# Kernel tuning notes

Hardware: AMD Instinct MI355X
Metric: run time of the kernel (lower is better)

## Reference

```python
import jax, jax.numpy as jnp
import numpy as np

N = 8192       # tokens = batch x seq
D = 2048       # d_model
H = 2048       # per-expert hidden size
E = 8          # num_experts
TOP_K = 2


def setup_inputs() -> dict:
    key = jax.random.key(0)
    ks = jax.random.split(key, 6)
    x = jax.random.normal(ks[0], (N, D), dtype=jnp.float32)
    expert_weights = jax.random.uniform(ks[1], (N, TOP_K), dtype=jnp.float32)
    expert_indices = jax.random.randint(ks[2], (N, TOP_K), 0, E, dtype=jnp.int32)
    batch_size_per_expert = jnp.bincount(expert_indices.reshape(-1), length=E).astype(jnp.int32)
    scale = 0.02
    w1 = jax.random.normal(ks[3], (E, D, H), dtype=jnp.float32) * scale
    w2 = jax.random.normal(ks[4], (E, H, D), dtype=jnp.float32) * scale
    w3 = jax.random.normal(ks[5], (E, D, H), dtype=jnp.float32) * scale
    return {"x": x, "expert_weights": expert_weights, "expert_indices": expert_indices,
            "batch_size_per_expert": batch_size_per_expert, "w1": w1, "w2": w2, "w3": w3}


def reference(x, expert_weights, expert_indices, batch_size_per_expert, w1, w2, w3):
    """Math-equivalent to ParallelMLP.forward_once (non-EP path):
    sort tokens by expert, run per-expert SwiGLU MLP, unpermute and combine
    with top-k routing weights. Output does not depend on the sort order,
    so we express it as: out[t] = sum_k w[t,k] * expert_{idx[t,k]}(x[t]).
    """
    n, d = x.shape
    e = w1.shape[0]
    # Dense combine weights (n, E): scatter top-k routing weights.
    cw = jnp.zeros((n, e), x.dtype).at[jnp.arange(n)[:, None], expert_indices].add(expert_weights)
    out = jnp.zeros_like(x)
    for i in range(e):  # small fixed expert count
        h = jax.nn.silu(x @ w1[i]) * (x @ w3[i])  # (n, H) SwiGLU
        out = out + cw[:, i:i + 1] * (h @ w2[i])
    return out
```

## Files before the change

kernel.cpp:

```cpp
#include <hip/hip_runtime.h>
#include <stdint.h>

typedef unsigned short u16;
typedef __attribute__((ext_vector_type(8))) short s16x8;
typedef __attribute__((ext_vector_type(8))) unsigned short u16x8;
typedef __attribute__((ext_vector_type(4))) float f32x4;

#define N_TOK 8192
#define DDIM 2048
#define HDIM 2048
#define NEXP 8
#define NROWS 16384
#define MAXTILES 136

#define W1T_OFF    0ull
#define W3T_OFF    67108864ull
#define W2T_OFF    134217728ull
#define XBF_OFF    201326592ull
#define HBUF_OFF   234881024ull
#define RES_OFF    301989888ull
#define ROWTOK_OFF 369098752ull
#define POS_OFF    369168384ull
#define META_OFF   369233920ull
#define WS_NEED    369234048ull

__device__ __forceinline__ u16 f2bf(float f) {
  union { float f; unsigned u; } v; v.f = f;
  unsigned r = v.u + 0x7fffu + ((v.u >> 16) & 1u);
  return (u16)(r >> 16);
}
__device__ __forceinline__ float bf2f(u16 u) {
  union { unsigned u; float f; } v; v.u = ((unsigned)u) << 16; return v.f;
}
__device__ __forceinline__ void gload_lds16(const u16* g, u16* l) {
  __builtin_amdgcn_global_load_lds(
      (const __attribute__((address_space(1))) unsigned int*)g,
      (__attribute__((address_space(3))) unsigned int*)l, 16, 0, 0);
}

__global__ void r1_kernel(const int* __restrict__ bsz, int* __restrict__ meta,
                          int* __restrict__ rowtok) {
  if (threadIdx.x == 0) {
    int off = 0, tbv = 0;
    meta[8] = 0; meta[17] = 0;
    for (int e = 0; e < 8; ++e) {
      meta[e] = 0;
      int c = bsz[e];
      off += c;  meta[9 + e] = off;
      tbv += (c + 127) >> 7; meta[18 + e] = tbv;
    }
  }
  for (int p = 16384 + (int)threadIdx.x; p < 17408; p += 256) rowtok[p] = 0;
}

__global__ void r2_kernel(const int* __restrict__ eidx, int* __restrict__ meta,
                          int* __restrict__ rowtok, int* __restrict__ posOf) {
  int i = blockIdx.x * 256 + threadIdx.x;
  int e = eidx[i];
  int p = atomicAdd(&meta[e], 1);
  int row = meta[8 + e] + p;
  rowtok[row] = i >> 1;
  posOf[i] = row;
}

__global__ void convert_x_kernel(const float* __restrict__ x, u16* __restrict__ xbf) {
  long long c = blockIdx.x * 256 + threadIdx.x;
  const float4 v0 = *(const float4*)&x[c * 8];
  const float4 v1 = *(const float4*)&x[c * 8 + 4];
  u16x8 u;
  u[0] = f2bf(v0.x); u[1] = f2bf(v0.y); u[2] = f2bf(v0.z); u[3] = f2bf(v0.w);
  u[4] = f2bf(v1.x); u[5] = f2bf(v1.y); u[6] = f2bf(v1.z); u[7] = f2bf(v1.w);
  *(u16x8*)&xbf[c * 8] = u;
}

__global__ __launch_bounds__(256) void transpose_cvt_kernel(
    const float* __restrict__ w1, const float* __restrict__ w2, const float* __restrict__ w3,
    u16* __restrict__ w1T, u16* __restrict__ w2T, u16* __restrict__ w3T) {
  __shared__ float tile[64][65];
  int z = blockIdx.z;
  const float* src; u16* dst;
  if (z < 8)        { src = w1 + (size_t)z * 4194304;        dst = w1T + (size_t)z * 4194304; }
  else if (z < 16)  { src = w3 + (size_t)(z - 8) * 4194304;  dst = w3T + (size_t)(z - 8) * 4194304; }
  else              { src = w2 + (size_t)(z - 16) * 4194304; dst = w2T + (size_t)(z - 16) * 4194304; }
  int r0 = blockIdx.y * 64, c0 = blockIdx.x * 64;
  int tid = threadIdx.x;
  int lr = tid >> 4, lc4 = (tid & 15) * 4;
#pragma unroll
  for (int i = 0; i < 4; ++i) {
    const float4 v = *(const float4*)&src[(size_t)(r0 + lr + i * 16) * 2048 + c0 + lc4];
    tile[lr + i * 16][lc4 + 0] = v.x; tile[lr + i * 16][lc4 + 1] = v.y;
    tile[lr + i * 16][lc4 + 2] = v.z; tile[lr + i * 16][lc4 + 3] = v.w;
  }
  __syncthreads();
  int orb = tid >> 3, oc8 = (tid & 7) * 8;
#pragma unroll
  for (int i = 0; i < 2; ++i) {
    int orow = orb + i * 32;
    u16x8 u;
#pragma unroll
    for (int j = 0; j < 8; ++j) u[j] = f2bf(tile[oc8 + j][orow]);
    *(u16x8*)&dst[(size_t)(c0 + orow) * 2048 + r0 + oc8] = u;
  }
}

__global__ __launch_bounds__(256, 2) void gemm1_kernel(
    const u16* __restrict__ xbf, const u16* __restrict__ w1T, const u16* __restrict__ w3T,
    const int* __restrict__ rowtok, const int* __restrict__ meta, u16* __restrict__ hbuf) {
  const int* offs = meta + 8;
  const int* tb = meta + 17;
  const int tileId = blockIdx.x;
  if (tileId >= tb[8]) return;
  int e = 0;
#pragma unroll
  for (int q = 1; q < 8; ++q) if (tileId >= tb[q]) e = q;
  const int row0 = offs[e] + (tileId - tb[e]) * 128;
  const int vr = offs[e + 1] - row0;
  const int n0 = blockIdx.y * 128;

  __shared__ u16 lds[2][3][128 * 32];

  const int tid = threadIdx.x;
  const int wv = tid >> 6, lane = tid & 63;
  const int ra0 = tid >> 2, ca0 = (tid & 3) * 8;
  const int tokA0 = rowtok[row0 + ra0];
  const int tokA1 = rowtok[row0 + ra0 + 64];
  const u16* aS0 = xbf + (size_t)tokA0 * DDIM + ca0;
  const u16* aS1 = xbf + (size_t)tokA1 * DDIM + ca0;
  const u16* b1S0 = w1T + ((size_t)e * HDIM + n0 + ra0) * DDIM + ca0;
  const u16* b1S1 = b1S0 + (size_t)64 * DDIM;
  const u16* b3S0 = w3T + ((size_t)e * HDIM + n0 + ra0) * DDIM + ca0;
  const u16* b3S1 = b3S0 + (size_t)64 * DDIM;
  const int wub0 = wv * 512, wub1 = 2048 + wv * 512;

  f32x4 zero4 = {0.f, 0.f, 0.f, 0.f};
  f32x4 acc1[4][4], acc3[4][4];
#pragma unroll
  for (int m = 0; m < 4; ++m)
#pragma unroll
    for (int n = 0; n < 4; ++n) { acc1[m][n] = zero4; acc3[m][n] = zero4; }

#define STAGE1(bufi, kt) do { int k0_ = (kt) * 32; \
    gload_lds16(aS0 + k0_,  &lds[bufi][0][wub0]); \
    gload_lds16(aS1 + k0_,  &lds[bufi][0][wub1]); \
    gload_lds16(b1S0 + k0_, &lds[bufi][1][wub0]); \
    gload_lds16(b1S1 + k0_, &lds[bufi][1][wub1]); \
    gload_lds16(b3S0 + k0_, &lds[bufi][2][wub0]); \
    gload_lds16(b3S1 + k0_, &lds[bufi][2][wub1]); } while (0)

  STAGE1(0, 0);
  __syncthreads();

  const int lm = lane & 15, kg = lane >> 4;
  const int wr = (wv >> 1) * 64, wc = (wv & 1) * 64;

  for (int kt = 0; kt < 64; ++kt) {
    const int cur = kt & 1;
    if (kt + 1 < 64) STAGE1(cur ^ 1, kt + 1);
    s16x8 a[4], b1[4], b3[4];
#pragma unroll
    for (int m = 0; m < 4; ++m)
      a[m] = *(const s16x8*)&lds[cur][0][(wr + m * 16 + lm) * 32 + kg * 8];
#pragma unroll
    for (int n = 0; n < 4; ++n) {
      b1[n] = *(const s16x8*)&lds[cur][1][(wc + n * 16 + lm) * 32 + kg * 8];
      b3[n] = *(const s16x8*)&lds[cur][2][(wc + n * 16 + lm) * 32 + kg * 8];
    }
#pragma unroll
    for (int m = 0; m < 4; ++m)
#pragma unroll
      for (int n = 0; n < 4; ++n) {
        acc1[m][n] = __builtin_amdgcn_mfma_f32_16x16x32_bf16(a[m], b1[n], acc1[m][n], 0, 0, 0);
        acc3[m][n] = __builtin_amdgcn_mfma_f32_16x16x32_bf16(a[m], b3[n], acc3[m][n], 0, 0, 0);
      }
    __syncthreads();
  }

#pragma unroll
  for (int m = 0; m < 4; ++m)
#pragma unroll
    for (int n = 0; n < 4; ++n) {
      f32x4 v1 = acc1[m][n], v3 = acc3[m][n];
      int col = n0 + wc + n * 16 + lm;
#pragma unroll
      for (int r = 0; r < 4; ++r) {
        int row = wr + m * 16 + kg * 4 + r;
        if (row < vr) {
          float z = v1[r];
          float hval = z / (1.f + __expf(-z)) * v3[r];
          hbuf[(size_t)(row0 + row) * HDIM + col] = f2bf(hval);
        }
      }
    }
#undef STAGE1
}

__global__ __launch_bounds__(256, 2) void gemm2_kernel(
    const u16* __restrict__ hbuf, const u16* __restrict__ w2T,
    const int* __restrict__ meta, u16* __restrict__ res) {
  const int* offs = meta + 8;
  const int* tb = meta + 17;
  const int tileId = blockIdx.x;
  if (tileId >= tb[8]) return;
  int e = 0;
#pragma unroll
  for (int q = 1; q < 8; ++q) if (tileId >= tb[q]) e = q;
  const int row0 = offs[e] + (tileId - tb[e]) * 128;
  const int vr = offs[e + 1] - row0;
  const int n0 = blockIdx.y * 128;

  __shared__ u16 lds[2][2][128 * 32];

  const int tid = threadIdx.x;
  const int wv = tid >> 6, lane = tid & 63;
  const int ra0 = tid >> 2, ca0 = (tid & 3) * 8;
  const u16* aS0 = hbuf + (size_t)(row0 + ra0) * HDIM + ca0;
  const u16* aS1 = aS0 + (size_t)64 * HDIM;
  const u16* bS0 = w2T + ((size_t)e * DDIM + n0 + ra0) * HDIM + ca0;
  const u16* bS1 = bS0 + (size_t)64 * HDIM;
  const int wub0 = wv * 512, wub1 = 2048 + wv * 512;

  f32x4 zero4 = {0.f, 0.f, 0.f, 0.f};
  f32x4 acc[4][4];
#pragma unroll
  for (int m = 0; m < 4; ++m)
#pragma unroll
    for (int n = 0; n < 4; ++n) acc[m][n] = zero4;

#define STAGE2(bufi, kt) do { int k0_ = (kt) * 32; \
    gload_lds16(aS0 + k0_, &lds[bufi][0][wub0]); \
    gload_lds16(aS1 + k0_, &lds[bufi][0][wub1]); \
    gload_lds16(bS0 + k0_, &lds[bufi][1][wub0]); \
    gload_lds16(bS1 + k0_, &lds[bufi][1][wub1]); } while (0)

  STAGE2(0, 0);
  __syncthreads();

  const int lm = lane & 15, kg = lane >> 4;
  const int wr = (wv >> 1) * 64, wc = (wv & 1) * 64;

  for (int kt = 0; kt < 64; ++kt) {
    const int cur = kt & 1;
    if (kt + 1 < 64) STAGE2(cur ^ 1, kt + 1);
    s16x8 a[4], b[4];
#pragma unroll
    for (int m = 0; m < 4; ++m)
      a[m] = *(const s16x8*)&lds[cur][0][(wr + m * 16 + lm) * 32 + kg * 8];
#pragma unroll
    for (int n = 0; n < 4; ++n)
      b[n] = *(const s16x8*)&lds[cur][1][(wc + n * 16 + lm) * 32 + kg * 8];
#pragma unroll
    for (int m = 0; m < 4; ++m)
#pragma unroll
      for (int n = 0; n < 4; ++n)
        acc[m][n] = __builtin_amdgcn_mfma_f32_16x16x32_bf16(a[m], b[n], acc[m][n], 0, 0, 0);
    __syncthreads();
  }

#pragma unroll
  for (int m = 0; m < 4; ++m)
#pragma unroll
    for (int n = 0; n < 4; ++n) {
      f32x4 v = acc[m][n];
      int col = n0 + wc + n * 16 + lm;
#pragma unroll
      for (int r = 0; r < 4; ++r) {
        int row = wr + m * 16 + kg * 4 + r;
        if (row < vr)
          res[(size_t)(row0 + row) * DDIM + col] = f2bf(v[r]);
      }
    }
#undef STAGE2
}

__global__ void combine_kernel(const u16* __restrict__ res, const int* __restrict__ posOf,
                               const float* __restrict__ ew, float* __restrict__ out) {
  int c = blockIdx.x * 256 + threadIdx.x;
  int t = c >> 8, dc = (c & 255) * 8;
  int p0 = posOf[2 * t], p1 = posOf[2 * t + 1];
  float wa = ew[2 * t], wb = ew[2 * t + 1];
  u16x8 u0 = *(const u16x8*)&res[(size_t)p0 * DDIM + dc];
  u16x8 u1 = *(const u16x8*)&res[(size_t)p1 * DDIM + dc];
  float4 o0, o1;
  o0.x = wa * bf2f(u0[0]) + wb * bf2f(u1[0]);
  o0.y = wa * bf2f(u0[1]) + wb * bf2f(u1[1]);
  o0.z = wa * bf2f(u0[2]) + wb * bf2f(u1[2]);
  o0.w = wa * bf2f(u0[3]) + wb * bf2f(u1[3]);
  o1.x = wa * bf2f(u0[4]) + wb * bf2f(u1[4]);
  o1.y = wa * bf2f(u0[5]) + wb * bf2f(u1[5]);
  o1.z = wa * bf2f(u0[6]) + wb * bf2f(u1[6]);
  o1.w = wa * bf2f(u0[7]) + wb * bf2f(u1[7]);
  *(float4*)&out[(size_t)t * DDIM + dc] = o0;
  *(float4*)&out[(size_t)t * DDIM + dc + 4] = o1;
}

extern "C" void kernel_launch(void* const* d_in, const int* in_sizes, int n_in,
                              void* d_out, int out_size, void* d_ws, size_t ws_size,
                              hipStream_t stream) {
  const float* x  = (const float*)d_in[0];
  const float* ew = (const float*)d_in[1];
  const int* eidx = (const int*)d_in[2];
  const int* bsz  = (const int*)d_in[3];
  const float* w1 = (const float*)d_in[4];
  const float* w2 = (const float*)d_in[5];
  const float* w3 = (const float*)d_in[6];
  float* out = (float*)d_out;
  char* ws = (char*)d_ws;

  if (ws_size < WS_NEED) {
    hipMemsetAsync(d_out, 0, (size_t)out_size * 4, stream);
    return;
  }

  u16* w1T = (u16*)(ws + W1T_OFF);
  u16* w3T = (u16*)(ws + W3T_OFF);
  u16* w2T = (u16*)(ws + W2T_OFF);
  u16* xbf = (u16*)(ws + XBF_OFF);
  u16* hbuf = (u16*)(ws + HBUF_OFF);
  u16* res = (u16*)(ws + RES_OFF);
  int* rowtok = (int*)(ws + ROWTOK_OFF);
  int* posOf = (int*)(ws + POS_OFF);
  int* meta = (int*)(ws + META_OFF);

  r1_kernel<<<1, 256, 0, stream>>>(bsz, meta, rowtok);
  r2_kernel<<<64, 256, 0, stream>>>(eidx, meta, rowtok, posOf);
  convert_x_kernel<<<8192, 256, 0, stream>>>(x, xbf);
  transpose_cvt_kernel<<<dim3(32, 32, 24), 256, 0, stream>>>(w1, w2, w3, w1T, w2T, w3T);
  gemm1_kernel<<<dim3(MAXTILES, 16), 256, 0, stream>>>(xbf, w1T, w3T, rowtok, meta, hbuf);
  gemm2_kernel<<<dim3(MAXTILES, 16), 256, 0, stream>>>(hbuf, w2T, meta, res);
  combine_kernel<<<8192, 256, 0, stream>>>(res, posOf, ew, out);
}
```

Measured before the change: 824.1 us.

## Replace MoE GEMMs with 256x256 8-wave templated kernel and XCD-aware tile mapping

Both expert GEMMs now share one templated kernel with 512 threads, 256-row tiles, K-step 64, XOR-swizzled LDS layout and a ping-pong schedule that interleaves prefetch, barriers and setprio around MFMA phases. Block ids are remapped so consecutive tiles land on the same XCD for better L2 reuse. The down-projection treats two 128-column halves as the B1/B3 operands to get a 256-wide output tile. The result buffer is aliased onto the dead w1T region to shrink the workspace. In exchange, padding per expert grows to 256 rows, which wastes more MFMA work on partial tiles.

```diff
diff --git a/kernel.cpp b/kernel.cpp
--- a/kernel.cpp
+++ b/kernel.cpp
@@ -9,20 +9,21 @@
 #define N_TOK 8192
 #define DDIM 2048
 #define HDIM 2048
-#define NEXP 8
 #define NROWS 16384
-#define MAXTILES 136
+#define PADROWS 16640
+#define MAXTILES 72
+#define KTILES 32
 
 #define W1T_OFF    0ull
 #define W3T_OFF    67108864ull
 #define W2T_OFF    134217728ull
 #define XBF_OFF    201326592ull
-#define HBUF_OFF   234881024ull
-#define RES_OFF    301989888ull
-#define ROWTOK_OFF 369098752ull
-#define POS_OFF    369168384ull
-#define META_OFF   369233920ull
-#define WS_NEED    369234048ull
+#define HS_OFF     234881024ull
+#define ROWTOK_OFF 303038464ull
+#define POS_OFF    303107072ull
+#define META_OFF   303172608ull
+#define RES_OFF    0ull
+#define WS_NEED    303172736ull
 
 __device__ __forceinline__ u16 f2bf(float f) {
   union { float f; unsigned u; } v; v.f = f;
@@ -47,10 +48,10 @@
       meta[e] = 0;
       int c = bsz[e];
       off += c;  meta[9 + e] = off;
-      tbv += (c + 127) >> 7; meta[18 + e] = tbv;
+      tbv += (c + 255) >> 8; meta[18 + e] = tbv;
     }
   }
-  for (int p = 16384 + (int)threadIdx.x; p < 17408; p += 256) rowtok[p] = 0;
+  for (int p = NROWS + (int)threadIdx.x; p < PADROWS; p += 256) rowtok[p] = 0;
 }
 
 __global__ void r2_kernel(const int* __restrict__ eidx, int* __restrict__ meta,
@@ -103,173 +104,195 @@
   }
 }
 
-__global__ __launch_bounds__(256, 2) void gemm1_kernel(
-    const u16* __restrict__ xbf, const u16* __restrict__ w1T, const u16* __restrict__ w3T,
-    const int* __restrict__ rowtok, const int* __restrict__ meta, u16* __restrict__ hbuf) {
+template<int EPI>
+__global__ __launch_bounds__(512, 2) void gemm_moe_kernel(
+    const u16* __restrict__ A, const u16* __restrict__ B1m, const u16* __restrict__ B3m,
+    const int* __restrict__ gather, const int* __restrict__ meta, u16* __restrict__ out) {
   const int* offs = meta + 8;
   const int* tb = meta + 17;
-  const int tileId = blockIdx.x;
+
+  const int nwg = (int)(gridDim.x * gridDim.y);
+  const int lin = (int)(blockIdx.y * gridDim.x + blockIdx.x);
+  const int q8 = nwg >> 3, r8 = nwg & 7;
+  const int xcd = lin & 7, idx = lin >> 3;
+  const int nl = (xcd < r8 ? xcd * (q8 + 1) : r8 * (q8 + 1) + (xcd - r8) * q8) + idx;
+  const int tileId = nl % MAXTILES;
+  const int colb = nl / MAXTILES;
+
   if (tileId >= tb[8]) return;
   int e = 0;
 #pragma unroll
-  for (int q = 1; q < 8; ++q) if (tileId >= tb[q]) e = q;
-  const int row0 = offs[e] + (tileId - tb[e]) * 128;
+  for (int qq = 1; qq < 8; ++qq) if (tileId >= tb[qq]) e = qq;
+  const int row0 = offs[e] + (tileId - tb[e]) * 256;
   const int vr = offs[e + 1] - row0;
-  const int n0 = blockIdx.y * 128;
-
-  __shared__ u16 lds[2][3][128 * 32];
+
+  const int bRowA = EPI ? colb * 128 : colb * 256;
+  const int bRowB = EPI ? colb * 128 : colb * 256 + 128;
+
+  __shared__ u16 lds[2][4][8192];
 
   const int tid = threadIdx.x;
-  const int wv = tid >> 6, lane = tid & 63;
-  const int ra0 = tid >> 2, ca0 = (tid & 3) * 8;
-  const int tokA0 = rowtok[row0 + ra0];
-  const int tokA1 = rowtok[row0 + ra0 + 64];
-  const u16* aS0 = xbf + (size_t)tokA0 * DDIM + ca0;
-  const u16* aS1 = xbf + (size_t)tokA1 * DDIM + ca0;
-  const u16* b1S0 = w1T + ((size_t)e * HDIM + n0 + ra0) * DDIM + ca0;
-  const u16* b1S1 = b1S0 + (size_t)64 * DDIM;
-  const u16* b3S0 = w3T + ((size_t)e * HDIM + n0 + ra0) * DDIM + ca0;
-  const u16* b3S1 = b3S0 + (size_t)64 * DDIM;
-  const int wub0 = wv * 512, wub1 = 2048 + wv * 512;
-
-  f32x4 zero4 = {0.f, 0.f, 0.f, 0.f};
-  f32x4 acc1[4][4], acc3[4][4];
-#pragma unroll
-  for (int m = 0; m < 4; ++m)
-#pragma unroll
-    for (int n = 0; n < 4; ++n) { acc1[m][n] = zero4; acc3[m][n] = zero4; }
-
-#define STAGE1(bufi, kt) do { int k0_ = (kt) * 32; \
-    gload_lds16(aS0 + k0_,  &lds[bufi][0][wub0]); \
-    gload_lds16(aS1 + k0_,  &lds[bufi][0][wub1]); \
-    gload_lds16(b1S0 + k0_, &lds[bufi][1][wub0]); \
-    gload_lds16(b1S1 + k0_, &lds[bufi][1][wub1]); \
-    gload_lds16(b3S0 + k0_, &lds[bufi][2][wub0]); \
-    gload_lds16(b3S1 + k0_, &lds[bufi][2][wub1]); } while (0)
-
-  STAGE1(0, 0);
-  __syncthreads();
-
+  const int wid = tid >> 6, lane = tid & 63;
   const int lm = lane & 15, kg = lane >> 4;
-  const int wr = (wv >> 1) * 64, wc = (wv & 1) * 64;
-
-  for (int kt = 0; kt < 64; ++kt) {
-    const int cur = kt & 1;
-    if (kt + 1 < 64) STAGE1(cur ^ 1, kt + 1);
-    s16x8 a[4], b1[4], b3[4];
-#pragma unroll
-    for (int m = 0; m < 4; ++m)
-      a[m] = *(const s16x8*)&lds[cur][0][(wr + m * 16 + lm) * 32 + kg * 8];
-#pragma unroll
-    for (int n = 0; n < 4; ++n) {
-      b1[n] = *(const s16x8*)&lds[cur][1][(wc + n * 16 + lm) * 32 + kg * 8];
-      b3[n] = *(const s16x8*)&lds[cur][2][(wc + n * 16 + lm) * 32 + kg * 8];
+  const int wr = wid >> 2, wc = wid & 3;
+
+  const u16* pA0[2]; const u16* pA1[2]; const u16* pB1[2]; const u16* pB3[2];
+#pragma unroll
+  for (int l = 0; l < 2; ++l) {
+    int S = (wid * 2 + l) * 64 + lane;
+    int r = S >> 3;
+    int c8 = ((S & 7) ^ (r & 7)) * 8;
+    int ga0 = row0 + r, ga1 = row0 + 128 + r;
+    int ta0 = gather ? gather[ga0] : ga0;
+    int ta1 = gather ? gather[ga1] : ga1;
+    pA0[l] = A + (size_t)ta0 * 2048 + c8;
+    pA1[l] = A + (size_t)ta1 * 2048 + c8;
+    pB1[l] = B1m + ((size_t)e * 2048 + bRowA + r) * 2048 + c8;
+    pB3[l] = B3m + ((size_t)e * 2048 + bRowB + r) * 2048 + c8;
+  }
+
+  int fA[2];
+  fA[0] = lm * 64 + ((kg) ^ (lm & 7)) * 8;
+  fA[1] = lm * 64 + ((4 + kg) ^ (lm & 7)) * 8;
+
+  f32x4 acc1[8][2], acc3[8][2];
+  f32x4 z4 = {0.f, 0.f, 0.f, 0.f};
+#pragma unroll
+  for (int m = 0; m < 8; ++m)
+#pragma unroll
+    for (int n = 0; n < 2; ++n) { acc1[m][n] = z4; acc3[m][n] = z4; }
+
+#define STG(b, u, P) do { \
+    gload_lds16(P[0], &lds[b][u][(wid * 2 + 0) * 512]); \
+    gload_lds16(P[1], &lds[b][u][(wid * 2 + 1) * 512]); } while (0)
+#define ADV() do { pA0[0]+=64; pA0[1]+=64; pA1[0]+=64; pA1[1]+=64; \
+    pB1[0]+=64; pB1[1]+=64; pB3[0]+=64; pB3[1]+=64; } while (0)
+
+  STG(0, 0, pA0); STG(0, 1, pA1); STG(0, 2, pB1); STG(0, 3, pB3);
+  ADV();
+  asm volatile("s_waitcnt vmcnt(0)" ::: "memory");
+  __builtin_amdgcn_s_barrier();
+
+  s16x8 a[4][2], b[2][2];
+
+  for (int t = 0; t < KTILES; ++t) {
+    const int cur = t & 1;
+    const bool more = (t + 1 < KTILES);
+
+#pragma unroll
+    for (int mi = 0; mi < 4; ++mi)
+#pragma unroll
+      for (int kk = 0; kk < 2; ++kk)
+        a[mi][kk] = *(const s16x8*)&lds[cur][wr][mi * 1024 + fA[kk]];
+#pragma unroll
+    for (int n = 0; n < 2; ++n)
+#pragma unroll
+      for (int kk = 0; kk < 2; ++kk)
+        b[n][kk] = *(const s16x8*)&lds[cur][2][wc * 2048 + n * 1024 + fA[kk]];
+    if (more) { STG(cur ^ 1, 0, pA0); STG(cur ^ 1, 2, pB1); }
+    __builtin_amdgcn_s_barrier();
+    __builtin_amdgcn_s_setprio(1);
+#pragma unroll
+    for (int mi = 0; mi < 4; ++mi)
+#pragma unroll
+      for (int n = 0; n < 2; ++n) {
+        acc1[mi][n] = __builtin_amdgcn_mfma_f32_16x16x32_bf16(a[mi][0], b[n][0], acc1[mi][n], 0, 0, 0);
+        acc1[mi][n] = __builtin_amdgcn_mfma_f32_16x16x32_bf16(a[mi][1], b[n][1], acc1[mi][n], 0, 0, 0);
+      }
+    __builtin_amdgcn_s_setprio(0);
+    __builtin_amdgcn_s_barrier();
+
+#pragma unroll
+    for (int n = 0; n < 2; ++n)
+#pragma unroll
+      for (int kk = 0; kk < 2; ++kk)
+        b[n][kk] = *(const s16x8*)&lds[cur][3][wc * 2048 + n * 1024 + fA[kk]];
+    if (more) { STG(cur ^ 1, 1, pA1); STG(cur ^ 1, 3, pB3); }
+    __builtin_amdgcn_s_barrier();
+    __builtin_amdgcn_s_setprio(1);
+#pragma unroll
+    for (int mi = 0; mi < 4; ++mi)
+#pragma unroll
+      for (int n = 0; n < 2; ++n) {
+        acc3[mi][n] = __builtin_amdgcn_mfma_f32_16x16x32_bf16(a[mi][0], b[n][0], acc3[mi][n], 0, 0, 0);
+        acc3[mi][n] = __builtin_amdgcn_mfma_f32_16x16x32_bf16(a[mi][1], b[n][1], acc3[mi][n], 0, 0, 0);
+      }
+    __builtin_amdgcn_s_setprio(0);
+    __builtin_amdgcn_s_barrier();
+
+#pragma unroll
+    for (int mi = 0; mi < 4; ++mi)
+#pragma unroll
+      for (int kk = 0; kk < 2; ++kk)
+        a[mi][kk] = *(const s16x8*)&lds[cur][wr][(4 + mi) * 1024 + fA[kk]];
+#pragma unroll
+    for (int n = 0; n < 2; ++n)
+#pragma unroll
+      for (int kk = 0; kk < 2; ++kk)
+        b[n][kk] = *(const s16x8*)&lds[cur][2][wc * 2048 + n * 1024 + fA[kk]];
+    __builtin_amdgcn_s_barrier();
+    __builtin_amdgcn_s_setprio(1);
+#pragma unroll
+    for (int mi = 0; mi < 4; ++mi)
+#pragma unroll
+      for (int n = 0; n < 2; ++n) {
+        acc1[4 + mi][n] = __builtin_amdgcn_mfma_f32_16x16x32_bf16(a[mi][0], b[n][0], acc1[4 + mi][n], 0, 0, 0);
+        acc1[4 + mi][n] = __builtin_amdgcn_mfma_f32_16x16x32_bf16(a[mi][1], b[n][1], acc1[4 + mi][n], 0, 0, 0);
+      }
+    __builtin_amdgcn_s_setprio(0);
+    __builtin_amdgcn_s_barrier();
+
+#pragma unroll
+    for (int n = 0; n < 2; ++n)
+#pragma unroll
+      for (int kk = 0; kk < 2; ++kk)
+        b[n][kk] = *(const s16x8*)&lds[cur][3][wc * 2048 + n * 1024 + fA[kk]];
+    asm volatile("s_waitcnt vmcnt(0)" ::: "memory");
+    __builtin_amdgcn_s_barrier();
+    __builtin_amdgcn_s_setprio(1);
+#pragma unroll
+    for (int mi = 0; mi < 4; ++mi)
+#pragma unroll
+      for (int n = 0; n < 2; ++n) {
+        acc3[4 + mi][n] = __builtin_amdgcn_mfma_f32_16x16x32_bf16(a[mi][0], b[n][0], acc3[4 + mi][n], 0, 0, 0);
+        acc3[4 + mi][n] = __builtin_amdgcn_mfma_f32_16x16x32_bf16(a[mi][1], b[n][1], acc3[4 + mi][n], 0, 0, 0);
+      }
+    __builtin_amdgcn_s_setprio(0);
+    __builtin_amdgcn_s_barrier();
+
+    if (more) ADV();
+  }
+
+#pragma unroll
+  for (int m = 0; m < 8; ++m)
+#pragma unroll
+    for (int n = 0; n < 2; ++n) {
+      const int rloc = wr * 128 + m * 16 + kg * 4;
+      if (EPI == 1) {
+        const int col = colb * 128 + wc * 32 + n * 16 + lm;
+#pragma unroll
+        for (int rr = 0; rr < 4; ++rr) {
+          int rowl = rloc + rr;
+          if (rowl < vr) {
+            float z = acc1[m][n][rr];
+            float h = z / (1.f + __expf(-z)) * acc3[m][n][rr];
+            out[(size_t)(row0 + rowl) * 2048 + col] = f2bf(h);
+          }
+        }
+      } else {
+        const int col = colb * 256 + wc * 32 + n * 16 + lm;
+#pragma unroll
+        for (int rr = 0; rr < 4; ++rr) {
+          int rowl = rloc + rr;
+          if (rowl < vr) {
+            out[(size_t)(row0 + rowl) * 2048 + col] = f2bf(acc1[m][n][rr]);
+            out[(size_t)(row0 + rowl) * 2048 + col + 128] = f2bf(acc3[m][n][rr]);
+          }
+        }
+      }
     }
-#pragma unroll
-    for (int m = 0; m < 4; ++m)
-#pragma unroll
-      for (int n = 0; n < 4; ++n) {
-        acc1[m][n] = __builtin_amdgcn_mfma_f32_16x16x32_bf16(a[m], b1[n], acc1[m][n], 0, 0, 0);
-        acc3[m][n] = __builtin_amdgcn_mfma_f32_16x16x32_bf16(a[m], b3[n], acc3[m][n], 0, 0, 0);
-      }
-    __syncthreads();
-  }
-
-#pragma unroll
-  for (int m = 0; m < 4; ++m)
-#pragma unroll
-    for (int n = 0; n < 4; ++n) {
-      f32x4 v1 = acc1[m][n], v3 = acc3[m][n];
-      int col = n0 + wc + n * 16 + lm;
-#pragma unroll
-      for (int r = 0; r < 4; ++r) {
-        int row = wr + m * 16 + kg * 4 + r;
-        if (row < vr) {
-          float z = v1[r];
-          float hval = z / (1.f + __expf(-z)) * v3[r];
-          hbuf[(size_t)(row0 + row) * HDIM + col] = f2bf(hval);
-        }
-      }
-    }
-#undef STAGE1
-}
-
-__global__ __launch_bounds__(256, 2) void gemm2_kernel(
-    const u16* __restrict__ hbuf, const u16* __restrict__ w2T,
-    const int* __restrict__ meta, u16* __restrict__ res) {
-  const int* offs = meta + 8;
-  const int* tb = meta + 17;
-  const int tileId = blockIdx.x;
-  if (tileId >= tb[8]) return;
-  int e = 0;
-#pragma unroll
-  for (int q = 1; q < 8; ++q) if (tileId >= tb[q]) e = q;
-  const int row0 = offs[e] + (tileId - tb[e]) * 128;
-  const int vr = offs[e + 1] - row0;
-  const int n0 = blockIdx.y * 128;
-
-  __shared__ u16 lds[2][2][128 * 32];
-
-  const int tid = threadIdx.x;
-  const int wv = tid >> 6, lane = tid & 63;
-  const int ra0 = tid >> 2, ca0 = (tid & 3) * 8;
-  const u16* aS0 = hbuf + (size_t)(row0 + ra0) * HDIM + ca0;
-  const u16* aS1 = aS0 + (size_t)64 * HDIM;
-  const u16* bS0 = w2T + ((size_t)e * DDIM + n0 + ra0) * HDIM + ca0;
-  const u16* bS1 = bS0 + (size_t)64 * HDIM;
-  const int wub0 = wv * 512, wub1 = 2048 + wv * 512;
-
-  f32x4 zero4 = {0.f, 0.f, 0.f, 0.f};
-  f32x4 acc[4][4];
-#pragma unroll
-  for (int m = 0; m < 4; ++m)
-#pragma unroll
-    for (int n = 0; n < 4; ++n) acc[m][n] = zero4;
-
-#define STAGE2(bufi, kt) do { int k0_ = (kt) * 32; \
-    gload_lds16(aS0 + k0_, &lds[bufi][0][wub0]); \
-    gload_lds16(aS1 + k0_, &lds[bufi][0][wub1]); \
-    gload_lds16(bS0 + k0_, &lds[bufi][1][wub0]); \
-    gload_lds16(bS1 + k0_, &lds[bufi][1][wub1]); } while (0)
-
-  STAGE2(0, 0);
-  __syncthreads();
-
-  const int lm = lane & 15, kg = lane >> 4;
-  const int wr = (wv >> 1) * 64, wc = (wv & 1) * 64;
-
-  for (int kt = 0; kt < 64; ++kt) {
-    const int cur = kt & 1;
-    if (kt + 1 < 64) STAGE2(cur ^ 1, kt + 1);
-    s16x8 a[4], b[4];
-#pragma unroll
-    for (int m = 0; m < 4; ++m)
-      a[m] = *(const s16x8*)&lds[cur][0][(wr + m * 16 + lm) * 32 + kg * 8];
-#pragma unroll
-    for (int n = 0; n < 4; ++n)
-      b[n] = *(const s16x8*)&lds[cur][1][(wc + n * 16 + lm) * 32 + kg * 8];
-#pragma unroll
-    for (int m = 0; m < 4; ++m)
-#pragma unroll
-      for (int n = 0; n < 4; ++n)
-        acc[m][n] = __builtin_amdgcn_mfma_f32_16x16x32_bf16(a[m], b[n], acc[m][n], 0, 0, 0);
-    __syncthreads();
-  }
-
-#pragma unroll
-  for (int m = 0; m < 4; ++m)
-#pragma unroll
-    for (int n = 0; n < 4; ++n) {
-      f32x4 v = acc[m][n];
-      int col = n0 + wc + n * 16 + lm;
-#pragma unroll
-      for (int r = 0; r < 4; ++r) {
-        int row = wr + m * 16 + kg * 4 + r;
-        if (row < vr)
-          res[(size_t)(row0 + row) * DDIM + col] = f2bf(v[r]);
-      }
-    }
-#undef STAGE2
+#undef STG
+#undef ADV
 }
 
 __global__ void combine_kernel(const u16* __restrict__ res, const int* __restrict__ posOf,
@@ -278,8 +301,8 @@
   int t = c >> 8, dc = (c & 255) * 8;
   int p0 = posOf[2 * t], p1 = posOf[2 * t + 1];
   float wa = ew[2 * t], wb = ew[2 * t + 1];
-  u16x8 u0 = *(const u16x8*)&res[(size_t)p0 * DDIM + dc];
-  u16x8 u1 = *(const u16x8*)&res[(size_t)p1 * DDIM + dc];
+  u16x8 u0 = *(const u16x8*)&res[(size_t)p0 * 2048 + dc];
+  u16x8 u1 = *(const u16x8*)&res[(size_t)p1 * 2048 + dc];
   float4 o0, o1;
   o0.x = wa * bf2f(u0[0]) + wb * bf2f(u1[0]);
   o0.y = wa * bf2f(u0[1]) + wb * bf2f(u1[1]);
@@ -289,8 +312,8 @@
   o1.y = wa * bf2f(u0[5]) + wb * bf2f(u1[5]);
   o1.z = wa * bf2f(u0[6]) + wb * bf2f(u1[6]);
   o1.w = wa * bf2f(u0[7]) + wb * bf2f(u1[7]);
-  *(float4*)&out[(size_t)t * DDIM + dc] = o0;
-  *(float4*)&out[(size_t)t * DDIM + dc + 4] = o1;
+  *(float4*)&out[(size_t)t * 2048 + dc] = o0;
+  *(float4*)&out[(size_t)t * 2048 + dc + 4] = o1;
 }
 
 extern "C" void kernel_launch(void* const* d_in, const int* in_sizes, int n_in,
@@ -315,17 +338,17 @@
   u16* w3T = (u16*)(ws + W3T_OFF);
   u16* w2T = (u16*)(ws + W2T_OFF);
   u16* xbf = (u16*)(ws + XBF_OFF);
-  u16* hbuf = (u16*)(ws + HBUF_OFF);
+  u16* hs  = (u16*)(ws + HS_OFF);
   u16* res = (u16*)(ws + RES_OFF);
   int* rowtok = (int*)(ws + ROWTOK_OFF);
-  int* posOf = (int*)(ws + POS_OFF);
-  int* meta = (int*)(ws + META_OFF);
+  int* posOf  = (int*)(ws + POS_OFF);
+  int* meta   = (int*)(ws + META_OFF);
 
   r1_kernel<<<1, 256, 0, stream>>>(bsz, meta, rowtok);
   r2_kernel<<<64, 256, 0, stream>>>(eidx, meta, rowtok, posOf);
   convert_x_kernel<<<8192, 256, 0, stream>>>(x, xbf);
   transpose_cvt_kernel<<<dim3(32, 32, 24), 256, 0, stream>>>(w1, w2, w3, w1T, w2T, w3T);
-  gemm1_kernel<<<dim3(MAXTILES, 16), 256, 0, stream>>>(xbf, w1T, w3T, rowtok, meta, hbuf);
-  gemm2_kernel<<<dim3(MAXTILES, 16), 256, 0, stream>>>(hbuf, w2T, meta, res);
+  gemm_moe_kernel<1><<<dim3(MAXTILES, 16), 512, 0, stream>>>(xbf, w1T, w3T, rowtok, meta, hs);
+  gemm_moe_kernel<0><<<dim3(MAXTILES, 8), 512, 0, stream>>>(hs, w2T, w2T, nullptr, meta, res);
   combine_kernel<<<8192, 256, 0, stream>>>(res, posOf, ew, out);
 }
```

Result: faster. 762.9 us (-7.4%).
